# Kernel tuning notes

Hardware: AMD Instinct MI355X
Metric: run time of the kernel (lower is better)

Reference implementation:

```python
import jax, jax.numpy as jnp
import numpy as np
from jax import lax

N, C, M = 512, 81, 28
NMS_THRESH = 0.5
EPS = 1e-4


def setup_inputs() -> dict:
    key = jax.random.key(0)
    k1, k2, k3, k4 = jax.random.split(key, 4)
    return {
        "left_logits": jax.random.normal(k1, (N, C, M, M), dtype=jnp.float32),
        "right_logits": jax.random.normal(k2, (N, C, M, M), dtype=jnp.float32),
        "scores": jax.random.uniform(k3, (N,), dtype=jnp.float32),
        "labels": jax.random.randint(k4, (N,), 0, C),
    }


def mask_nms_keep(probs, scores, thresh):
    # probs: [N, M, M] float mask probabilities; greedy suppression in score order.
    n = probs.shape[0]
    order = jnp.argsort(-scores)
    P = probs[order].reshape(n, -1)                  # [N, M*M] sorted by score desc
    inter = P @ P.T                                   # pairwise sum(mask_i * mask_j)
    u = P.sum(-1)                                     # per-mask area (numerator mask only)
    iou = inter / (u[:, None] + EPS)                  # asymmetric IoU as in mask_iou()
    upper = jnp.triu(jnp.ones((n, n), dtype=bool), 1) # j > i

    def body(i, suppressed):
        sup_row = (~suppressed[i]) & upper[i] & (iou[i] >= thresh)
        return suppressed | sup_row

    suppressed = lax.fori_loop(0, n, body, jnp.zeros(n, dtype=bool))
    keep_sorted = ~suppressed
    # map back to original detection order
    return jnp.zeros(n, dtype=bool).at[order].set(keep_sorted)


def reference(left_logits, right_logits, scores, labels):
    idx = jnp.arange(left_logits.shape[0])
    # full-tensor sigmoid then per-class gather, as in the original module
    left_prob = jax.nn.sigmoid(left_logits)[idx, labels][:, None]    # [N,1,M,M]
    right_prob = jax.nn.sigmoid(right_logits)[idx, labels][:, None]  # [N,1,M,M]

    # filter_empty: both sides must have nonzero mask mass
    valid = (left_prob[:, 0].sum((-1, -2)) > 0) & (right_prob[:, 0].sum((-1, -2)) > 0)

    left_keep = mask_nms_keep(left_prob[:, 0], scores, NMS_THRESH)
    right_keep = mask_nms_keep(right_prob[:, 0], scores, NMS_THRESH)
    keep = valid & left_keep & right_keep  # intersection of left/right NMS keeps

    probs = jnp.stack([left_prob, right_prob], axis=0)  # [2,N,1,M,M]
    return probs, keep
```

## Files before the change

kernel.cpp:

```cpp
#include <hip/hip_runtime.h>
#include <math.h>

#define NDET 512
#define NCLS 81
#define MM   784
#define PROBS_ELEMS (2 * NDET * MM)
#define NMS_TH 0.5
#define EPS_D  1e-4
#define SD 116

typedef double dbl4 __attribute__((ext_vector_type(4)));


__global__ __launch_bounds__(256) void k12_fused(
    const float* __restrict__ left, const float* __restrict__ right,
    const float* __restrict__ scores, const int* __restrict__ labels,
    float* __restrict__ out, double* __restrict__ u, int* __restrict__ order) {
  if (blockIdx.x == 256) {
    __shared__ float sk[NDET];
    __shared__ int   si[NDET];
    int t = threadIdx.x;
    for (int e = t; e < NDET; e += 256) { sk[e] = scores[e]; si[e] = e; }
    __syncthreads();
    for (int k = 2; k <= NDET; k <<= 1) {
      for (int j = k >> 1; j > 0; j >>= 1) {
        for (int e = t; e < NDET; e += 256) {
          int p = e ^ j;
          if (p > e) {
            bool dir = ((e & k) == 0);
            float sa = sk[e], sb = sk[p];
            int ia = si[e], ib = si[p];
            bool aBeforeB = (sa > sb) || (sa == sb && ia < ib);
            bool doSwap = dir ? (!aBeforeB) : aBeforeB;
            if (doSwap) { sk[e] = sb; si[e] = ib; sk[p] = sa; si[p] = ia; }
          }
        }
        __syncthreads();
      }
    }
    for (int e = t; e < NDET; e += 256) order[e] = si[e];
    return;
  }

  int wv = threadIdx.x >> 6;
  int lane = threadIdx.x & 63;
  int m = (blockIdx.x << 2) | wv;
  int s = m >> 9;
  int n = m & 511;
  const float* src = (s == 0) ? left : right;
  int lab = labels[n];
  const float4* in4 = (const float4*)(src + ((size_t)n * NCLS + lab) * MM);
  float4* out4 = (float4*)(out + ((size_t)s * NDET + n) * MM);
  double local = 0.0;
  for (int i = lane; i < MM / 4; i += 64) {
    float4 v = in4[i];
    float4 r;
    r.x = 1.0f / (1.0f + expf(-v.x));
    r.y = 1.0f / (1.0f + expf(-v.y));
    r.z = 1.0f / (1.0f + expf(-v.z));
    r.w = 1.0f / (1.0f + expf(-v.w));
    out4[i] = r;
    local += (double)r.x + (double)r.y + (double)r.z + (double)r.w;
  }
#pragma unroll
  for (int off = 32; off > 0; off >>= 1)
    local += __shfl_down(local, off, 64);
  if (lane == 0) u[s * NDET + n] = local;
}

__global__ __launch_bounds__(256) void k3_iou(
    const float* __restrict__ P,
    const double* __restrict__ u,
    const int* __restrict__ order,
    unsigned int* __restrict__ bits32) {
  int bi = blockIdx.x;
  int s = bi / 136;
  int tri = bi % 136;
  int ti = 0, rem = tri;
  while (rem >= 16 - ti) { rem -= 16 - ti; ti++; }
  int tj = ti + rem;

  __shared__ __align__(16) float As[32][SD];
  __shared__ __align__(16) float Bs[32][SD];
  __shared__ int oi[32], oj[32];
  __shared__ double den05[32];
  __shared__ unsigned char pred[32][32];

  int t = threadIdx.x;
  if (t < 32) {
    int r = order[ti * 32 + t];
    oi[t] = r;
    den05[t] = 0.5 * (u[s * NDET + r] + EPS_D);
    oj[t] = order[tj * 32 + t];
  }
  __syncthreads();

  const float* Pside = P + (size_t)s * NDET * MM;

  const float4* gsrc[7];
  float* ldst[7];
#pragma unroll
  for (int i = 0; i < 7; i++) {
    int idx = t + 256 * i;
    int ab = (idx >= 896);
    int idc = ab ? (idx - 896) : idx;
    int r = idc / 28;
    int c4 = idc - r * 28;
    int o = ab ? oj[r] : oi[r];
    gsrc[i] = (const float4*)(Pside + (size_t)o * MM) + c4;
    ldst[i] = ab ? &Bs[r][4 * c4] : &As[r][4 * c4];
  }

  float4 pf[7];
#pragma unroll
  for (int i = 0; i < 7; i++) pf[i] = gsrc[i][0];

  int wv = t >> 6;
  int lane = t & 63;
  int qi = (wv >> 1) & 1;
  int qj = wv & 1;
  int fr = lane & 15;
  int fk = lane >> 4;
  const float* aF = &As[qi * 16 + fr][fk];
  const float* bF = &Bs[qj * 16 + fr][fk];

  double ap = (fk == 0) ? 1.0 : (fk == 1) ? (double)fr : 0.0;
  double bp = (fk == 0) ? (double)fr : (fk == 1) ? 16.0 : 0.0;
  dbl4 dp = {0.0, 0.0, 0.0, 0.0};
  dp = __builtin_amdgcn_mfma_f64_16x16x4f64(ap, bp, dp, 0, 0, 0);

  dbl4 acc0 = {0.0, 0.0, 0.0, 0.0};
  dbl4 acc1 = {0.0, 0.0, 0.0, 0.0};

  for (int kc = 0; kc < 7; kc++) {
#pragma unroll
    for (int i = 0; i < 7; i++) *(float4*)ldst[i] = pf[i];
    __syncthreads();
    if (kc < 6) {
#pragma unroll
      for (int i = 0; i < 7; i++) pf[i] = gsrc[i][(kc + 1) * 28];
    }
#pragma unroll
    for (int st = 0; st < 28; st += 2) {
      double a0 = (double)aF[st * 4];
      double b0 = (double)bF[st * 4];
      acc0 = __builtin_amdgcn_mfma_f64_16x16x4f64(a0, b0, acc0, 0, 0, 0);
      double a1 = (double)aF[(st + 1) * 4];
      double b1 = (double)bF[(st + 1) * 4];
      acc1 = __builtin_amdgcn_mfma_f64_16x16x4f64(a1, b1, acc1, 0, 0, 0);
    }
    __syncthreads();
  }

#pragma unroll
  for (int r = 0; r < 4; r++) {
    int code = (int)dp[r];
    int di = code >> 4;
    int dj = code & 15;
    double v = acc0[r] + acc1[r];
    bool p = (v >= den05[qi * 16 + di]);
    pred[qi * 16 + di][qj * 16 + dj] = p ? 1 : 0;
  }
  __syncthreads();

  if (t < 32) {
    unsigned m = 0;
#pragma unroll
    for (int c = 0; c < 32; c++) m |= ((unsigned)pred[t][c]) << c;
    bits32[((size_t)s * NDET + ti * 32 + t) * 16 + tj] = m;
  }
}

__global__ __launch_bounds__(512) void k4_greedy(
    const unsigned long long* __restrict__ bits,
    const int* __restrict__ order,
    const double* __restrict__ u,
    float* __restrict__ outKeep) {
  __shared__ unsigned long long B[2 * NDET * 8];
  __shared__ unsigned char keepO[2 * NDET];
  int t = threadIdx.x;

  for (int e = t; e < 2 * NDET * 8; e += 512) {
    unsigned long long w = bits[e];
    int g = e & 7;
    int i = (e >> 3) & 511;
    int gi = i >> 6;
    if (g < gi) {
      w = 0ull;
    } else if (g == gi) {
      int li = i & 63;
      w = (li == 63) ? 0ull : (w & (~0ull << (li + 1)));
    }
    B[e] = w;
  }
  __syncthreads();

  int wv = t >> 6;
  int lane = t & 63;
  if (wv < 2) {
    int s = wv;
    const unsigned long long* Bside = B + (size_t)s * NDET * 8;
    unsigned long long S0 = 0, S1 = 0, S2 = 0, S3 = 0,
                       S4 = 0, S5 = 0, S6 = 0, S7 = 0;

#define GROUP(G, SG, ORS)                                              \
    for (int li = 0; li < 64; li++) {                                  \
      unsigned act = (unsigned)((SG >> li) & 1ull);                    \
      if (__builtin_amdgcn_readfirstlane(act) == 0) {                  \
        const unsigned long long* row = Bside + ((((G) << 6) | li) << 3); \
        ORS                                                            \
      }                                                                \
    }
    GROUP(0, S0, { S0 |= row[0]; S1 |= row[1]; S2 |= row[2]; S3 |= row[3];
                   S4 |= row[4]; S5 |= row[5]; S6 |= row[6]; S7 |= row[7]; })
    GROUP(1, S1, { S1 |= row[1]; S2 |= row[2]; S3 |= row[3];
                   S4 |= row[4]; S5 |= row[5]; S6 |= row[6]; S7 |= row[7]; })
    GROUP(2, S2, { S2 |= row[2]; S3 |= row[3];
                   S4 |= row[4]; S5 |= row[5]; S6 |= row[6]; S7 |= row[7]; })
    GROUP(3, S3, { S3 |= row[3];
                   S4 |= row[4]; S5 |= row[5]; S6 |= row[6]; S7 |= row[7]; })
    GROUP(4, S4, { S4 |= row[4]; S5 |= row[5]; S6 |= row[6]; S7 |= row[7]; })
    GROUP(5, S5, { S5 |= row[5]; S6 |= row[6]; S7 |= row[7]; })
    GROUP(6, S6, { S6 |= row[6]; S7 |= row[7]; })
    GROUP(7, S7, { S7 |= row[7]; })
#undef GROUP

    unsigned long long Sarr[8] = {S0, S1, S2, S3, S4, S5, S6, S7};
#pragma unroll
    for (int g = 0; g < 8; g++) {
      int c = (g << 6) | lane;
      keepO[s * NDET + order[c]] =
          (unsigned char)(((Sarr[g] >> lane) & 1ull) ^ 1ull);
    }
  }
  __syncthreads();

  if (t < NDET) {
    bool valid = (u[t] > 0.0) && (u[NDET + t] > 0.0);
    outKeep[t] = (valid && keepO[t] && keepO[NDET + t]) ? 1.0f : 0.0f;
  }
}

extern "C" void kernel_launch(void* const* d_in, const int* in_sizes, int n_in,
                              void* d_out, int out_size, void* d_ws, size_t ws_size,
                              hipStream_t stream) {
  const float* left   = (const float*)d_in[0];
  const float* right  = (const float*)d_in[1];
  const float* scores = (const float*)d_in[2];
  const int*   labels = (const int*)d_in[3];
  float* out = (float*)d_out;

  char* ws = (char*)d_ws;
  double* u                = (double*)(ws + 0);
  int* order               = (int*)(ws + 8192);
  unsigned int* bits32     = (unsigned int*)(ws + 16384);
  unsigned long long* bits = (unsigned long long*)(ws + 16384);

  k12_fused<<<257, 256, 0, stream>>>(left, right, scores, labels, out, u, order);
  k3_iou<<<272, 256, 0, stream>>>(out, u, order, bits32);
  k4_greedy<<<1, 512, 0, stream>>>(bits, order, u, out + PROBS_ELEMS);
}
```

Before: 296.6 us.

## Replace FP64 MFMA IoU tile with split-K scalar FMA register tiling

The IoU tile kernel drops the f64 MFMA instructions. Each wave now computes a 4x4 register tile over a quarter of the K dimension using scalar double FMAs. Shared tiles are stored pre-converted to double, and the four wave partials are reduced through a new shared buffer before thresholding. This removes the per-element float-to-double conversions in the inner loop and the MFMA layout decode. The cost is more shared memory (about 29KB for the two double tiles plus about 25KB for the partials), lower occupancy, and use of the vector ALU instead of the matrix cores.

```diff
diff --git a/kernel.cpp b/kernel.cpp
--- a/kernel.cpp
+++ b/kernel.cpp
@@ -7,9 +7,7 @@
 #define PROBS_ELEMS (2 * NDET * MM)
 #define NMS_TH 0.5
 #define EPS_D  1e-4
-#define SD 116
-
-typedef double dbl4 __attribute__((ext_vector_type(4)));
+#define SDD 114
 
 
 __global__ __launch_bounds__(256) void k12_fused(
@@ -80,8 +78,9 @@
   while (rem >= 16 - ti) { rem -= 16 - ti; ti++; }
   int tj = ti + rem;
 
-  __shared__ __align__(16) float As[32][SD];
-  __shared__ __align__(16) float Bs[32][SD];
+  __shared__ __align__(16) double Asd[32][SDD];
+  __shared__ __align__(16) double Bsd[32][SDD];
+  __shared__ double Cp[3][32][33];
   __shared__ int oi[32], oj[32];
   __shared__ double den05[32];
   __shared__ unsigned char pred[32][32];
@@ -98,7 +97,7 @@
   const float* Pside = P + (size_t)s * NDET * MM;
 
   const float4* gsrc[7];
-  float* ldst[7];
+  double* ldst[7];
 #pragma unroll
   for (int i = 0; i < 7; i++) {
     int idx = t + 256 * i;
@@ -108,7 +107,7 @@
     int c4 = idc - r * 28;
     int o = ab ? oj[r] : oi[r];
     gsrc[i] = (const float4*)(Pside + (size_t)o * MM) + c4;
-    ldst[i] = ab ? &Bs[r][4 * c4] : &As[r][4 * c4];
+    ldst[i] = ab ? &Bsd[r][4 * c4] : &Asd[r][4 * c4];
   }
 
   float4 pf[7];
@@ -117,52 +116,71 @@
 
   int wv = t >> 6;
   int lane = t & 63;
-  int qi = (wv >> 1) & 1;
-  int qj = wv & 1;
-  int fr = lane & 15;
-  int fk = lane >> 4;
-  const float* aF = &As[qi * 16 + fr][fk];
-  const float* bF = &Bs[qj * 16 + fr][fk];
-
-  double ap = (fk == 0) ? 1.0 : (fk == 1) ? (double)fr : 0.0;
-  double bp = (fk == 0) ? (double)fr : (fk == 1) ? 16.0 : 0.0;
-  dbl4 dp = {0.0, 0.0, 0.0, 0.0};
-  dp = __builtin_amdgcn_mfma_f64_16x16x4f64(ap, bp, dp, 0, 0, 0);
-
-  dbl4 acc0 = {0.0, 0.0, 0.0, 0.0};
-  dbl4 acc1 = {0.0, 0.0, 0.0, 0.0};
+  int tx = lane & 7;
+  int ty = (lane >> 3) & 7;
+  int kb = 28 * wv;
+
+  double acc[4][4];
+#pragma unroll
+  for (int i = 0; i < 4; i++)
+#pragma unroll
+    for (int j = 0; j < 4; j++) acc[i][j] = 0.0;
 
   for (int kc = 0; kc < 7; kc++) {
 #pragma unroll
-    for (int i = 0; i < 7; i++) *(float4*)ldst[i] = pf[i];
+    for (int i = 0; i < 7; i++) {
+      float4 v = pf[i];
+      double2 d0; d0.x = (double)v.x; d0.y = (double)v.y;
+      double2 d1; d1.x = (double)v.z; d1.y = (double)v.w;
+      *(double2*)(ldst[i])     = d0;
+      *(double2*)(ldst[i] + 2) = d1;
+    }
     __syncthreads();
     if (kc < 6) {
 #pragma unroll
       for (int i = 0; i < 7; i++) pf[i] = gsrc[i][(kc + 1) * 28];
     }
 #pragma unroll
-    for (int st = 0; st < 28; st += 2) {
-      double a0 = (double)aF[st * 4];
-      double b0 = (double)bF[st * 4];
-      acc0 = __builtin_amdgcn_mfma_f64_16x16x4f64(a0, b0, acc0, 0, 0, 0);
-      double a1 = (double)aF[(st + 1) * 4];
-      double b1 = (double)bF[(st + 1) * 4];
-      acc1 = __builtin_amdgcn_mfma_f64_16x16x4f64(a1, b1, acc1, 0, 0, 0);
+    for (int kp = 0; kp < 14; kp++) {
+      double2 av[4], bv[4];
+#pragma unroll
+      for (int i = 0; i < 4; i++)
+        av[i] = *(const double2*)&Asd[ty + 8 * i][kb + 2 * kp];
+#pragma unroll
+      for (int j = 0; j < 4; j++)
+        bv[j] = *(const double2*)&Bsd[tx + 8 * j][kb + 2 * kp];
+#pragma unroll
+      for (int i = 0; i < 4; i++)
+#pragma unroll
+        for (int j = 0; j < 4; j++) {
+          acc[i][j] = fma(av[i].x, bv[j].x, acc[i][j]);
+          acc[i][j] = fma(av[i].y, bv[j].y, acc[i][j]);
+        }
     }
     __syncthreads();
   }
 
-#pragma unroll
-  for (int r = 0; r < 4; r++) {
-    int code = (int)dp[r];
-    int di = code >> 4;
-    int dj = code & 15;
-    double v = acc0[r] + acc1[r];
-    bool p = (v >= den05[qi * 16 + di]);
-    pred[qi * 16 + di][qj * 16 + dj] = p ? 1 : 0;
-  }
-  __syncthreads();
-
+  if (wv > 0) {
+#pragma unroll
+    for (int i = 0; i < 4; i++)
+#pragma unroll
+      for (int j = 0; j < 4; j++)
+        Cp[wv - 1][ty + 8 * i][tx + 8 * j] = acc[i][j];
+  }
+  __syncthreads();
+  if (wv == 0) {
+#pragma unroll
+    for (int i = 0; i < 4; i++) {
+      int r = ty + 8 * i;
+#pragma unroll
+      for (int j = 0; j < 4; j++) {
+        int c = tx + 8 * j;
+        double v = acc[i][j] + Cp[0][r][c] + Cp[1][r][c] + Cp[2][r][c];
+        pred[r][c] = (v >= den05[r]) ? 1 : 0;
+      }
+    }
+  }
+  __syncthreads();
   if (t < 32) {
     unsigned m = 0;
 #pragma unroll
```

Result: faster. 285.9 us (-3.6%).
